# Kernel optimization log

Measured on AMD Instinct MI355X. Metric: run time of the kernel, lower is better.

Reference implementation:

```python
import jax, jax.numpy as jnp
import numpy as np

N, E = 100000, 3200000          # nodes, edges
D_IN, HID, OUT = 128, 128, 64   # in_channels, hidden_channels, out_channels
EPS = 1e-5                      # BatchNorm1d eps


def setup_inputs() -> dict:
    key = jax.random.key(0)
    ks = jax.random.split(key, 16)
    s = 0.05
    return {
        "x": jax.random.normal(ks[0], (N, D_IN), jnp.float32),
        "edge_index": jax.random.randint(ks[1], (2, E), 0, N, dtype=jnp.int64),
        # layer 0 (first_aggr=True): lin_pos_l (no bias), lin_pos_r (bias), lin_neg_r (bias)
        # (lin_neg_l acts on the all-zero neg aggregation -> contributes nothing, omitted)
        "w0_pos_l": jax.random.normal(ks[2], (HID, D_IN), jnp.float32) * s,
        "w0_pos_r": jax.random.normal(ks[3], (HID, D_IN), jnp.float32) * s,
        "b0_pos_r": jnp.zeros((HID,), jnp.float32),
        "w0_neg_r": jax.random.normal(ks[4], (HID, D_IN), jnp.float32) * s,
        "b0_neg_r": jnp.zeros((HID,), jnp.float32),
        # BatchNorm1d(2*HID)
        "bn_gamma": jnp.ones((2 * HID,), jnp.float32),
        "bn_beta": jnp.zeros((2 * HID,), jnp.float32),
        # layer 1 (first_aggr=False), in dim 2*HID split into pos/neg halves of HID.
        # Only the pos-edge aggregation block of lin_*_l is live (neg edges empty).
        "w1_pos_l": jax.random.normal(ks[5], (OUT, HID), jnp.float32) * s,
        "w1_pos_r": jax.random.normal(ks[6], (OUT, 2 * HID), jnp.float32) * s,
        "b1_pos_r": jnp.zeros((OUT,), jnp.float32),
        "w1_neg_l": jax.random.normal(ks[7], (OUT, HID), jnp.float32) * s,
        "w1_neg_r": jax.random.normal(ks[8], (OUT, 2 * HID), jnp.float32) * s,
        "b1_neg_r": jnp.zeros((OUT,), jnp.float32),
    }


def reference(x, edge_index, w0_pos_l, w0_pos_r, b0_pos_r, w0_neg_r, b0_neg_r,
              bn_gamma, bn_beta, w1_pos_l, w1_pos_r, b1_pos_r,
              w1_neg_l, w1_neg_r, b1_neg_r):
    src, dst = edge_index[0], edge_index[1]
    n = x.shape[0]
    deg = jax.ops.segment_sum(jnp.ones(src.shape, x.dtype), dst, num_segments=n)
    inv_deg = (1.0 / jnp.maximum(deg, 1.0))[:, None]

    def agg_mean(h):  # PyG mean aggregation over pos edges: src -> dst
        return jax.ops.segment_sum(h[src], dst, num_segments=n) * inv_deg

    # ---- layer 0: SignedConv(first_aggr=True); neg_edge_index is empty ----
    m = agg_mean(x)                                      # [N, D_IN]
    out_pos = m @ w0_pos_l.T + x @ w0_pos_r.T + b0_pos_r  # [N, HID]
    out_neg = x @ w0_neg_r.T + b0_neg_r                   # neg aggr == 0
    h = jnp.concatenate([out_pos, out_neg], axis=-1)      # [N, 2*HID]

    # ---- BatchNorm1d (batch statistics) + ReLU; dropout inactive (eval) ----
    mu = h.mean(axis=0)
    var = h.var(axis=0)
    h = (h - mu) * jax.lax.rsqrt(var + EPS) * bn_gamma + bn_beta
    h = jax.nn.relu(h)

    # ---- layer 1: SignedConv(first_aggr=False); neg edges empty ----
    f = h.shape[-1] // 2
    hp, hn = h[:, :f], h[:, f:]
    out_pos = agg_mean(hp) @ w1_pos_l.T + h @ w1_pos_r.T + b1_pos_r  # [N, OUT]
    out_neg = agg_mean(hn) @ w1_neg_l.T + h @ w1_neg_r.T + b1_neg_r  # [N, OUT]
    return jnp.concatenate([out_pos, out_neg], axis=-1)              # [N, 2*OUT]
```

## Files before the change

### kernel.cpp

```cpp
#include <hip/hip_runtime.h>
#include <stdint.h>

typedef __attribute__((ext_vector_type(8))) short short8;
typedef __attribute__((ext_vector_type(4))) float floatx4;

__device__ inline unsigned short f2bf(float f) {
    union { float f; unsigned u; } v; v.f = f;
    unsigned u = v.u;
    u += 0x7fffu + ((u >> 16) & 1u);
    return (unsigned short)(u >> 16);
}
__device__ inline unsigned char f2fp8(float f) {
    int r = __builtin_amdgcn_cvt_pk_fp8_f32(f, f, 0, false);
    return (unsigned char)(r & 0xff);
}

__global__ void k_detect(const unsigned* __restrict__ w, int* __restrict__ flag, int nwords) {
    unsigned a = 0;
    for (int i = 1 + 2 * (int)threadIdx.x; i < nwords; i += 512) a |= w[i];
    if (threadIdx.x == 0) *flag = 0;
    __syncthreads();
    if (a) *flag = 1;
}

__global__ void k_remap_hist(const void* __restrict__ ei_raw, const int* __restrict__ flag,
                             int* __restrict__ src, int* __restrict__ dst,
                             int* __restrict__ bhist, int E, int n, int NB) {
    __shared__ int lh[256];
    int t = threadIdx.x;
    if (t < 256) lh[t] = 0;
    __syncthreads();
    int base = blockIdx.x * 4096;
    bool is32 = (*flag != 0);
#pragma unroll
    for (int j = 0; j < 4; j++) {
        int e = base + j * 1024 + t;
        if (e < E) {
            int s, d;
            if (is32) { const int* p = (const int*)ei_raw; s = p[e]; d = p[E + e]; }
            else      { const long long* p = (const long long*)ei_raw; s = (int)p[e]; d = (int)p[E + e]; }
            s = s < 0 ? 0 : (s >= n ? n - 1 : s);
            d = d < 0 ? 0 : (d >= n ? n - 1 : d);
            src[e] = s; dst[e] = d;
            atomicAdd(&lh[d >> 9], 1);
        }
    }
    __syncthreads();
    if (t < NB && lh[t]) atomicAdd(&bhist[t], lh[t]);
}

__global__ void k_offsets(const int* __restrict__ bhist, int* __restrict__ bbase,
                          int* __restrict__ pcur, int* __restrict__ row_ptr,
                          int E, int n, int NB) {
    __shared__ int sc[256], orig[256];
    int t = threadIdx.x;
    int v = (t < NB) ? bhist[t] : 0;
    orig[t] = v; sc[t] = v;
    __syncthreads();
    for (int off = 1; off < 256; off <<= 1) {
        int x = (t >= off) ? sc[t - off] : 0;
        __syncthreads();
        sc[t] += x;
        __syncthreads();
    }
    if (t < NB) {
        int e = sc[t] - orig[t];
        bbase[t] = e; pcur[t] = e;
    }
    if (t == NB) bbase[t] = E;
    if (t == 0) row_ptr[n] = E;
}

__global__ void k_phase1(const int* __restrict__ src, const int* __restrict__ dst,
                         int* __restrict__ pcur, unsigned* __restrict__ pairs, int E, int NB) {
    __shared__ int lh[256];
    __shared__ int gbase[256];
    int t = threadIdx.x;
    if (t < 256) lh[t] = 0;
    __syncthreads();
    int base = blockIdx.x * 16384;
    int rank[16], dreg[16];
#pragma unroll
    for (int j = 0; j < 16; j++) {
        int e = base + j * 1024 + t;
        dreg[j] = -1;
        if (e < E) {
            int d = dst[e];
            dreg[j] = d;
            rank[j] = atomicAdd(&lh[d >> 9], 1);
        }
    }
    __syncthreads();
    if (t < NB && lh[t]) gbase[t] = atomicAdd(&pcur[t], lh[t]);
    __syncthreads();
#pragma unroll
    for (int j = 0; j < 16; j++) {
        int e = base + j * 1024 + t;
        if (e < E) {
            int s = src[e];
            int d = dreg[j];
            pairs[gbase[d >> 9] + rank[j]] = ((unsigned)s << 9) | (unsigned)(d & 511);
        }
    }
}

__global__ void k_phase2(const unsigned* __restrict__ pairs, const int* __restrict__ bbase,
                         int* __restrict__ row_ptr, float* __restrict__ inv_deg,
                         int* __restrict__ col, int n) {
    __shared__ int lcount[512];
    __shared__ int sc[512];
    __shared__ int lcur[512];
    int t = threadIdx.x;
    int b = blockIdx.x;
    lcount[t] = 0;
    __syncthreads();
    int e0 = bbase[b], e1 = bbase[b + 1];
    for (int i = e0 + t; i < e1; i += 512) {
        unsigned v = pairs[i];
        atomicAdd(&lcount[v & 511u], 1);
    }
    __syncthreads();
    sc[t] = lcount[t];
    __syncthreads();
    for (int off = 1; off < 512; off <<= 1) {
        int x = (t >= off) ? sc[t - off] : 0;
        __syncthreads();
        sc[t] += x;
        __syncthreads();
    }
    int excl = sc[t] - lcount[t];
    lcur[t] = excl;
    int g = b * 512 + t;
    if (g < n) {
        row_ptr[g] = e0 + excl;
        int c = lcount[t];
        inv_deg[g] = 1.0f / (float)(c > 1 ? c : 1);
    }
    __syncthreads();
    for (int i = e0 + t; i < e1; i += 512) {
        unsigned v = pairs[i];
        int f = v & 511u;
        int p = atomicAdd(&lcur[f], 1);
        col[e0 + p] = (int)(v >> 9);
    }
}

__global__ void k_w0prep(const float* __restrict__ wl, const float* __restrict__ wr,
                         const float* __restrict__ wn, unsigned short* __restrict__ W0f) {
    int tid = blockIdx.x * 256 + threadIdx.x;
    int lane = tid & 63; int ks = (tid >> 6) & 3; int ct = tid >> 8;
    int o = ct * 16 + (lane & 15);
    int k0 = ks * 32 + (lane >> 4) * 8;
    const float* sp = (o < 128) ? (wl + o * 128)
                    : (o < 256) ? (wr + (o - 128) * 128)
                                : (wn + (o - 256) * 128);
    union { unsigned short u[8]; short8 v; } pk;
#pragma unroll
    for (int j = 0; j < 8; j++) pk.u[j] = f2bf(sp[k0 + j]);
    ((short8*)W0f)[(ct * 4 + ks) * 64 + lane] = pk.v;
}

__global__ void k_w1prep(const float* __restrict__ wpl, const float* __restrict__ wnl,
                         const float* __restrict__ wpr, const float* __restrict__ wnr,
                         unsigned short* __restrict__ W1f) {
    int tid = blockIdx.x * 256 + threadIdx.x;
    int lane = tid & 63; int ks = (tid >> 6) & 7; int ct = tid >> 9;
    int o = ct * 16 + (lane & 15);
    int k0 = ks * 32 + (lane >> 4) * 8;
    union { unsigned short u[8]; short8 v; } pk;
#pragma unroll
    for (int j = 0; j < 8; j++) {
        int k = k0 + j;
        float v;
        if (o < 64)        v = (k < 128) ? wpl[o * 128 + k] : 0.0f;
        else if (o < 128)  v = (k >= 128) ? wnl[(o - 64) * 128 + (k - 128)] : 0.0f;
        else if (o < 192)  v = wpr[(o - 128) * 256 + k];
        else               v = wnr[(o - 192) * 256 + k];
        pk.u[j] = f2bf(v);
    }
    ((short8*)W1f)[(ct * 8 + ks) * 64 + lane] = pk.v;
}

__launch_bounds__(256, 2)
__global__ void k_gemm0(const float* __restrict__ x, const unsigned short* __restrict__ W0f,
                        const float* __restrict__ b0p, const float* __restrict__ b0n,
                        unsigned char* __restrict__ P, float* __restrict__ h, int n) {
    __shared__ unsigned short As[64 * 136];
    int t = threadIdx.x; int wave = t >> 6; int lane = t & 63;
    const short8* wf = (const short8*)W0f;
    short8 Bf[6][4];
#pragma unroll
    for (int i = 0; i < 6; i++) {
        int ct = wave * 6 + i;
#pragma unroll
        for (int ks = 0; ks < 4; ks++) Bf[i][ks] = wf[(ct * 4 + ks) * 64 + lane];
    }
    int rowbase = blockIdx.x * 64;
#pragma unroll
    for (int it = 0; it < 4; it++) {
        int seg = it * 256 + t;
        int r = seg >> 4; int k0 = (seg & 15) * 8;
        int row = rowbase + r;
        float4 a = {0, 0, 0, 0}, b = {0, 0, 0, 0};
        if (row < n) {
            a = *(const float4*)(x + (size_t)row * 128 + k0);
            b = *(const float4*)(x + (size_t)row * 128 + k0 + 4);
        }
        union { unsigned short u[8]; uint4 q; } pk;
        pk.u[0] = f2bf(a.x); pk.u[1] = f2bf(a.y); pk.u[2] = f2bf(a.z); pk.u[3] = f2bf(a.w);
        pk.u[4] = f2bf(b.x); pk.u[5] = f2bf(b.y); pk.u[6] = f2bf(b.z); pk.u[7] = f2bf(b.w);
        *(uint4*)(&As[r * 136 + k0]) = pk.q;
    }
    __syncthreads();
    int m = lane & 15; int quad = lane >> 4;
#pragma unroll
    for (int rt = 0; rt < 4; rt++) {
        floatx4 acc[6];
#pragma unroll
        for (int i = 0; i < 6; i++) acc[i] = (floatx4){0.f, 0.f, 0.f, 0.f};
#pragma unroll
        for (int ks = 0; ks < 4; ks++) {
            short8 a = *(const short8*)(&As[(rt * 16 + m) * 136 + ks * 32 + quad * 8]);
#pragma unroll
            for (int i = 0; i < 6; i++)
                acc[i] = __builtin_amdgcn_mfma_f32_16x16x32_bf16(a, Bf[i][ks], acc[i], 0, 0, 0);
        }
#pragma unroll
        for (int i = 0; i < 6; i++) {
            int colg = wave * 96 + i * 16 + m;
            float bias = 0.f;
            if (colg >= 128 && colg < 256) bias = b0p[colg - 128];
            else if (colg >= 256)          bias = b0n[colg - 256];
#pragma unroll
            for (int rr = 0; rr < 4; rr++) {
                int row = rowbase + rt * 16 + quad * 4 + rr;
                if (row < n) {
                    float v = acc[i][rr] + bias;
                    if (colg < 128) P[(size_t)row * 128 + colg] = f2fp8(v);
                    else            h[(size_t)row * 256 + (colg - 128)] = v;
                }
            }
        }
    }
}

template<int OSTRIDE>
__global__ __launch_bounds__(256) void k_agg(const int* __restrict__ row_ptr,
                                             const int* __restrict__ col,
                                             const float* __restrict__ inv_deg,
                                             const unsigned* __restrict__ Prow,
                                             float* __restrict__ out, int n) {
    int wid = threadIdx.x >> 6, lane = threadIdx.x & 63;
    int node = blockIdx.x * 4 + wid;
    if (node >= n) return;
    int e0 = row_ptr[node], e1 = row_ptr[node + 1];
    int half = lane >> 5, li = lane & 31;
    float a0 = 0.f, a1 = 0.f, a2 = 0.f, a3 = 0.f;
    for (int j = e0; j < e1; j += 64) {
        int cnt = e1 - j; if (cnt > 64) cnt = 64;
        int idx = j + lane;
        int myc = col[idx < e1 ? idx : e1 - 1];
        int i = 0;
        for (; i + 8 <= cnt; i += 8) {
            int sA = __shfl(myc, i + half);
            int sB = __shfl(myc, i + 2 + half);
            int sC = __shfl(myc, i + 4 + half);
            int sD = __shfl(myc, i + 6 + half);
            unsigned vA = Prow[(size_t)sA * 32 + li];
            unsigned vB = Prow[(size_t)sB * 32 + li];
            unsigned vC = Prow[(size_t)sC * 32 + li];
            unsigned vD = Prow[(size_t)sD * 32 + li];
            a0 += __builtin_amdgcn_cvt_f32_fp8(vA, 0); a1 += __builtin_amdgcn_cvt_f32_fp8(vA, 1);
            a2 += __builtin_amdgcn_cvt_f32_fp8(vA, 2); a3 += __builtin_amdgcn_cvt_f32_fp8(vA, 3);
            a0 += __builtin_amdgcn_cvt_f32_fp8(vB, 0); a1 += __builtin_amdgcn_cvt_f32_fp8(vB, 1);
            a2 += __builtin_amdgcn_cvt_f32_fp8(vB, 2); a3 += __builtin_amdgcn_cvt_f32_fp8(vB, 3);
            a0 += __builtin_amdgcn_cvt_f32_fp8(vC, 0); a1 += __builtin_amdgcn_cvt_f32_fp8(vC, 1);
            a2 += __builtin_amdgcn_cvt_f32_fp8(vC, 2); a3 += __builtin_amdgcn_cvt_f32_fp8(vC, 3);
            a0 += __builtin_amdgcn_cvt_f32_fp8(vD, 0); a1 += __builtin_amdgcn_cvt_f32_fp8(vD, 1);
            a2 += __builtin_amdgcn_cvt_f32_fp8(vD, 2); a3 += __builtin_amdgcn_cvt_f32_fp8(vD, 3);
        }
        for (; i + 2 <= cnt; i += 2) {
            int s = __shfl(myc, i + half);
            unsigned v = Prow[(size_t)s * 32 + li];
            a0 += __builtin_amdgcn_cvt_f32_fp8(v, 0); a1 += __builtin_amdgcn_cvt_f32_fp8(v, 1);
            a2 += __builtin_amdgcn_cvt_f32_fp8(v, 2); a3 += __builtin_amdgcn_cvt_f32_fp8(v, 3);
        }
        if (i < cnt) {
            int s = __shfl(myc, i);
            if (half == 0) {
                unsigned v = Prow[(size_t)s * 32 + li];
                a0 += __builtin_amdgcn_cvt_f32_fp8(v, 0); a1 += __builtin_amdgcn_cvt_f32_fp8(v, 1);
                a2 += __builtin_amdgcn_cvt_f32_fp8(v, 2); a3 += __builtin_amdgcn_cvt_f32_fp8(v, 3);
            }
        }
    }
    a0 += __shfl_xor(a0, 32);
    a1 += __shfl_xor(a1, 32);
    a2 += __shfl_xor(a2, 32);
    a3 += __shfl_xor(a3, 32);
    float idg = inv_deg[node];
    float rx = half ? a2 : a0;
    float ry = half ? a3 : a1;
    float* o = out + (size_t)node * OSTRIDE + 4 * li + 2 * half;
    float2 q = *(const float2*)o;
    float2 r;
    r.x = rx * idg + q.x;
    r.y = ry * idg + q.y;
    *(float2*)o = r;
}

__global__ void k_stats(const float* __restrict__ h, float* __restrict__ colsum,
                        float* __restrict__ colsumsq, int n) {
    int t = threadIdx.x;
    float s = 0.f, ss = 0.f;
    for (int r = blockIdx.x; r < n; r += gridDim.x) {
        float v = h[(size_t)r * 256 + t];
        s += v; ss += v * v;
    }
    atomicAdd(&colsum[t], s);
    atomicAdd(&colsumsq[t], ss);
}

__global__ void k_bnfin(const float* __restrict__ colsum, const float* __restrict__ colsumsq,
                        const float* __restrict__ gamma, const float* __restrict__ beta,
                        float* __restrict__ scale, float* __restrict__ shift, int n) {
    int t = threadIdx.x;
    float inv_n = 1.0f / (float)n;
    float mu = colsum[t] * inv_n;
    float var = colsumsq[t] * inv_n - mu * mu;
    float sc = gamma[t] * rsqrtf(var + 1e-5f);
    scale[t] = sc;
    shift[t] = beta[t] - mu * sc;
}

__launch_bounds__(256, 2)
__global__ void k_gemm1(const float* __restrict__ h, const unsigned short* __restrict__ W1f,
                        const float* __restrict__ bnscale, const float* __restrict__ bnshift,
                        const float* __restrict__ b1p, const float* __restrict__ b1n,
                        unsigned char* __restrict__ Y, float* __restrict__ out, int n) {
    __shared__ unsigned short As[64 * 264];
    __shared__ float sc[256], sh[256];
    int t = threadIdx.x; int wave = t >> 6; int lane = t & 63;
    sc[t] = bnscale[t]; sh[t] = bnshift[t];
    const short8* wf = (const short8*)W1f;
    short8 Bf[4][8];
#pragma unroll
    for (int i = 0; i < 4; i++) {
        int ct = wave * 4 + i;
#pragma unroll
        for (int ks = 0; ks < 8; ks++) Bf[i][ks] = wf[(ct * 8 + ks) * 64 + lane];
    }
    __syncthreads();
    int rowbase = blockIdx.x * 64;
#pragma unroll
    for (int it = 0; it < 8; it++) {
        int seg = it * 256 + t;
        int r = seg >> 5; int k0 = (seg & 31) * 8;
        int row = rowbase + r;
        union { unsigned short u[8]; uint4 q; } pk;
        if (row < n) {
            float4 a = *(const float4*)(h + (size_t)row * 256 + k0);
            float4 b = *(const float4*)(h + (size_t)row * 256 + k0 + 4);
            float vv[8] = {a.x, a.y, a.z, a.w, b.x, b.y, b.z, b.w};
#pragma unroll
            for (int q2 = 0; q2 < 8; q2++) {
                float v = vv[q2] * sc[k0 + q2] + sh[k0 + q2];
                v = v > 0.f ? v : 0.f;
                pk.u[q2] = f2bf(v);
            }
        } else {
#pragma unroll
            for (int q2 = 0; q2 < 8; q2++) pk.u[q2] = 0;
        }
        *(uint4*)(&As[r * 264 + k0]) = pk.q;
    }
    __syncthreads();
    int m = lane & 15; int quad = lane >> 4;
#pragma unroll
    for (int rt = 0; rt < 4; rt++) {
        floatx4 acc[4];
#pragma unroll
        for (int i = 0; i < 4; i++) acc[i] = (floatx4){0.f, 0.f, 0.f, 0.f};
#pragma unroll
        for (int ks = 0; ks < 8; ks++) {
            short8 a = *(const short8*)(&As[(rt * 16 + m) * 264 + ks * 32 + quad * 8]);
#pragma unroll
            for (int i = 0; i < 4; i++)
                acc[i] = __builtin_amdgcn_mfma_f32_16x16x32_bf16(a, Bf[i][ks], acc[i], 0, 0, 0);
        }
#pragma unroll
        for (int i = 0; i < 4; i++) {
            int colg = wave * 64 + i * 16 + m;
#pragma unroll
            for (int rr = 0; rr < 4; rr++) {
                int row = rowbase + rt * 16 + quad * 4 + rr;
                if (row < n) {
                    float v = acc[i][rr];
                    if (colg < 128) {
                        Y[(size_t)row * 128 + colg] = f2fp8(v);
                    } else {
                        float bias = (colg < 192) ? b1p[colg - 128] : b1n[colg - 192];
                        out[(size_t)row * 128 + (colg - 128)] = v + bias;
                    }
                }
            }
        }
    }
}

extern "C" void kernel_launch(void* const* d_in, const int* in_sizes, int n_in,
                              void* d_out, int out_size, void* d_ws, size_t ws_size,
                              hipStream_t stream) {
    const float* x        = (const float*)d_in[0];
    const void*  ei_raw   = d_in[1];
    const float* w0_pos_l = (const float*)d_in[2];
    const float* w0_pos_r = (const float*)d_in[3];
    const float* b0_pos_r = (const float*)d_in[4];
    const float* w0_neg_r = (const float*)d_in[5];
    const float* b0_neg_r = (const float*)d_in[6];
    const float* bn_gamma = (const float*)d_in[7];
    const float* bn_beta  = (const float*)d_in[8];
    const float* w1_pos_l = (const float*)d_in[9];
    const float* w1_pos_r = (const float*)d_in[10];
    const float* b1_pos_r = (const float*)d_in[11];
    const float* w1_neg_l = (const float*)d_in[12];
    const float* w1_neg_r = (const float*)d_in[13];
    const float* b1_neg_r = (const float*)d_in[14];
    float* out = (float*)d_out;
    int N = in_sizes[0] / 128;
    int E = in_sizes[1] / 2;
    int NB = (N + 511) >> 9;

    char* ws = (char*)d_ws;
    size_t off = 0;
    auto carve = [&](size_t bytes) -> char* {
        char* p = ws + off;
        off += (bytes + 255) & ~(size_t)255;
        return p;
    };
    int*      eflag   = (int*)carve(256);
    int*      src     = (int*)carve((size_t)E * 4);
    int*      dst     = (int*)carve((size_t)E * 4);
    int*      bhist   = (int*)carve((size_t)NB * 4);
    int*      bbase   = (int*)carve((size_t)(NB + 1) * 4);
    int*      pcur    = (int*)carve((size_t)NB * 4);
    int*      row_ptr = (int*)carve((size_t)(N + 1) * 4);
    float*    inv_deg = (float*)carve((size_t)N * 4);
    unsigned* pairs   = (unsigned*)carve((size_t)E * 4);
    int*      ecol    = (int*)carve((size_t)E * 4);
    unsigned char* P  = (unsigned char*)carve((size_t)N * 128);
    float* h          = (float*)carve((size_t)N * 256 * 4);
    unsigned char* Yb = (unsigned char*)carve((size_t)N * 128);
    unsigned short* W0f = (unsigned short*)carve(24 * 4 * 64 * 8 * 2);
    unsigned short* W1f = (unsigned short*)carve(16 * 8 * 64 * 8 * 2);
    float* colsum   = (float*)carve(2 * 256 * 4);
    float* colsumsq = colsum + 256;
    float* bnscale  = (float*)carve(256 * 4);
    float* bnshift  = (float*)carve(256 * 4);

    hipMemsetAsync(bhist, 0, (size_t)NB * 4, stream);
    hipMemsetAsync(colsum, 0, 2 * 256 * 4, stream);

    int nwords = 2 * E < 32768 ? 2 * E : 32768;
    k_detect<<<1, 256, 0, stream>>>((const unsigned*)ei_raw, eflag, nwords);
    k_remap_hist<<<(E + 4095) / 4096, 1024, 0, stream>>>(ei_raw, eflag, src, dst, bhist, E, N, NB);
    k_offsets<<<1, 256, 0, stream>>>(bhist, bbase, pcur, row_ptr, E, N, NB);
    k_phase1<<<(E + 16383) / 16384, 1024, 0, stream>>>(src, dst, pcur, pairs, E, NB);
    k_phase2<<<NB, 512, 0, stream>>>(pairs, bbase, row_ptr, inv_deg, ecol, N);

    k_w0prep<<<24, 256, 0, stream>>>(w0_pos_l, w0_pos_r, w0_neg_r, W0f);
    k_w1prep<<<32, 256, 0, stream>>>(w1_pos_l, w1_neg_l, w1_pos_r, w1_neg_r, W1f);

    int gb = (N + 63) / 64;
    k_gemm0<<<gb, 256, 0, stream>>>(x, W0f, b0_pos_r, b0_neg_r, P, h, N);
    k_agg<256><<<(N + 3) / 4, 256, 0, stream>>>(row_ptr, ecol, inv_deg, (const unsigned*)P, h, N);
    k_stats<<<256, 256, 0, stream>>>(h, colsum, colsumsq, N);
    k_bnfin<<<1, 256, 0, stream>>>(colsum, colsumsq, bn_gamma, bn_beta, bnscale, bnshift, N);
    k_gemm1<<<gb, 256, 0, stream>>>(h, W1f, bnscale, bnshift, b1_pos_r, b1_neg_r, Yb, out, N);
    k_agg<128><<<(N + 3) / 4, 256, 0, stream>>>(row_ptr, ecol, inv_deg, (const unsigned*)Yb, out, N);
}
```

Before: 606.6 us.

## Fuse BatchNorm column statistics into gemm0 and aggregation kernels

```diff
diff --git a/kernel.cpp b/kernel.cpp
--- a/kernel.cpp
+++ b/kernel.cpp
@@ -184,7 +184,8 @@
 __launch_bounds__(256, 2)
 __global__ void k_gemm0(const float* __restrict__ x, const unsigned short* __restrict__ W0f,
                         const float* __restrict__ b0p, const float* __restrict__ b0n,
-                        unsigned char* __restrict__ P, float* __restrict__ h, int n) {
+                        unsigned char* __restrict__ P, float* __restrict__ h,
+                        float* __restrict__ colsum, float* __restrict__ colsumsq, int n) {
     __shared__ unsigned short As[64 * 136];
     int t = threadIdx.x; int wave = t >> 6; int lane = t & 63;
     const short8* wf = (const short8*)W0f;
@@ -213,6 +214,9 @@
     }
     __syncthreads();
     int m = lane & 15; int quad = lane >> 4;
+    float cs[6], cq[6];
+#pragma unroll
+    for (int i = 0; i < 6; i++) { cs[i] = 0.f; cq[i] = 0.f; }
 #pragma unroll
     for (int rt = 0; rt < 4; rt++) {
         floatx4 acc[6];
@@ -236,89 +240,111 @@
                 int row = rowbase + rt * 16 + quad * 4 + rr;
                 if (row < n) {
                     float v = acc[i][rr] + bias;
-                    if (colg < 128) P[(size_t)row * 128 + colg] = f2fp8(v);
-                    else            h[(size_t)row * 256 + (colg - 128)] = v;
+                    if (colg < 128) {
+                        P[(size_t)row * 128 + colg] = f2fp8(v);
+                    } else {
+                        h[(size_t)row * 256 + (colg - 128)] = v;
+                        if (colg >= 256) { cs[i] += v; cq[i] += v * v; }
+                    }
                 }
             }
         }
     }
-}
-
-template<int OSTRIDE>
+#pragma unroll
+    for (int i = 0; i < 6; i++) {
+        int colg = wave * 96 + i * 16 + m;
+        if (colg >= 256) {
+            float s = cs[i];
+            s += __shfl_xor(s, 16); s += __shfl_xor(s, 32);
+            float q = cq[i];
+            q += __shfl_xor(q, 16); q += __shfl_xor(q, 32);
+            if (quad == 0) {
+                atomicAdd(&colsum[colg - 128], s);
+                atomicAdd(&colsumsq[colg - 128], q);
+            }
+        }
+    }
+}
+
+template<int OSTRIDE, bool STATS>
 __global__ __launch_bounds__(256) void k_agg(const int* __restrict__ row_ptr,
                                              const int* __restrict__ col,
                                              const float* __restrict__ inv_deg,
                                              const unsigned* __restrict__ Prow,
-                                             float* __restrict__ out, int n) {
+                                             float* __restrict__ out,
+                                             float* __restrict__ colsum,
+                                             float* __restrict__ colsumsq, int n) {
     int wid = threadIdx.x >> 6, lane = threadIdx.x & 63;
-    int node = blockIdx.x * 4 + wid;
-    if (node >= n) return;
-    int e0 = row_ptr[node], e1 = row_ptr[node + 1];
     int half = lane >> 5, li = lane & 31;
-    float a0 = 0.f, a1 = 0.f, a2 = 0.f, a3 = 0.f;
-    for (int j = e0; j < e1; j += 64) {
-        int cnt = e1 - j; if (cnt > 64) cnt = 64;
-        int idx = j + lane;
-        int myc = col[idx < e1 ? idx : e1 - 1];
-        int i = 0;
-        for (; i + 8 <= cnt; i += 8) {
-            int sA = __shfl(myc, i + half);
-            int sB = __shfl(myc, i + 2 + half);
-            int sC = __shfl(myc, i + 4 + half);
-            int sD = __shfl(myc, i + 6 + half);
-            unsigned vA = Prow[(size_t)sA * 32 + li];
-            unsigned vB = Prow[(size_t)sB * 32 + li];
-            unsigned vC = Prow[(size_t)sC * 32 + li];
-            unsigned vD = Prow[(size_t)sD * 32 + li];
-            a0 += __builtin_amdgcn_cvt_f32_fp8(vA, 0); a1 += __builtin_amdgcn_cvt_f32_fp8(vA, 1);
-            a2 += __builtin_amdgcn_cvt_f32_fp8(vA, 2); a3 += __builtin_amdgcn_cvt_f32_fp8(vA, 3);
-            a0 += __builtin_amdgcn_cvt_f32_fp8(vB, 0); a1 += __builtin_amdgcn_cvt_f32_fp8(vB, 1);
-            a2 += __builtin_amdgcn_cvt_f32_fp8(vB, 2); a3 += __builtin_amdgcn_cvt_f32_fp8(vB, 3);
-            a0 += __builtin_amdgcn_cvt_f32_fp8(vC, 0); a1 += __builtin_amdgcn_cvt_f32_fp8(vC, 1);
-            a2 += __builtin_amdgcn_cvt_f32_fp8(vC, 2); a3 += __builtin_amdgcn_cvt_f32_fp8(vC, 3);
-            a0 += __builtin_amdgcn_cvt_f32_fp8(vD, 0); a1 += __builtin_amdgcn_cvt_f32_fp8(vD, 1);
-            a2 += __builtin_amdgcn_cvt_f32_fp8(vD, 2); a3 += __builtin_amdgcn_cvt_f32_fp8(vD, 3);
-        }
-        for (; i + 2 <= cnt; i += 2) {
-            int s = __shfl(myc, i + half);
-            unsigned v = Prow[(size_t)s * 32 + li];
-            a0 += __builtin_amdgcn_cvt_f32_fp8(v, 0); a1 += __builtin_amdgcn_cvt_f32_fp8(v, 1);
-            a2 += __builtin_amdgcn_cvt_f32_fp8(v, 2); a3 += __builtin_amdgcn_cvt_f32_fp8(v, 3);
-        }
-        if (i < cnt) {
-            int s = __shfl(myc, i);
-            if (half == 0) {
+    float sx = 0.f, sy = 0.f, qx = 0.f, qy = 0.f;
+    for (int node = blockIdx.x * 4 + wid; node < n; node += gridDim.x * 4) {
+        int e0 = row_ptr[node], e1 = row_ptr[node + 1];
+        float a0 = 0.f, a1 = 0.f, a2 = 0.f, a3 = 0.f;
+        for (int j = e0; j < e1; j += 64) {
+            int cnt = e1 - j; if (cnt > 64) cnt = 64;
+            int idx = j + lane;
+            int myc = col[idx < e1 ? idx : e1 - 1];
+            int i = 0;
+            for (; i + 8 <= cnt; i += 8) {
+                int sA = __shfl(myc, i + half);
+                int sB = __shfl(myc, i + 2 + half);
+                int sC = __shfl(myc, i + 4 + half);
+                int sD = __shfl(myc, i + 6 + half);
+                unsigned vA = Prow[(size_t)sA * 32 + li];
+                unsigned vB = Prow[(size_t)sB * 32 + li];
+                unsigned vC = Prow[(size_t)sC * 32 + li];
+                unsigned vD = Prow[(size_t)sD * 32 + li];
+                a0 += __builtin_amdgcn_cvt_f32_fp8(vA, 0); a1 += __builtin_amdgcn_cvt_f32_fp8(vA, 1);
+                a2 += __builtin_amdgcn_cvt_f32_fp8(vA, 2); a3 += __builtin_amdgcn_cvt_f32_fp8(vA, 3);
+                a0 += __builtin_amdgcn_cvt_f32_fp8(vB, 0); a1 += __builtin_amdgcn_cvt_f32_fp8(vB, 1);
+                a2 += __builtin_amdgcn_cvt_f32_fp8(vB, 2); a3 += __builtin_amdgcn_cvt_f32_fp8(vB, 3);
+                a0 += __builtin_amdgcn_cvt_f32_fp8(vC, 0); a1 += __builtin_amdgcn_cvt_f32_fp8(vC, 1);
+                a2 += __builtin_amdgcn_cvt_f32_fp8(vC, 2); a3 += __builtin_amdgcn_cvt_f32_fp8(vC, 3);
+                a0 += __builtin_amdgcn_cvt_f32_fp8(vD, 0); a1 += __builtin_amdgcn_cvt_f32_fp8(vD, 1);
+                a2 += __builtin_amdgcn_cvt_f32_fp8(vD, 2); a3 += __builtin_amdgcn_cvt_f32_fp8(vD, 3);
+            }
+            for (; i + 2 <= cnt; i += 2) {
+                int s = __shfl(myc, i + half);
                 unsigned v = Prow[(size_t)s * 32 + li];
                 a0 += __builtin_amdgcn_cvt_f32_fp8(v, 0); a1 += __builtin_amdgcn_cvt_f32_fp8(v, 1);
                 a2 += __builtin_amdgcn_cvt_f32_fp8(v, 2); a3 += __builtin_amdgcn_cvt_f32_fp8(v, 3);
             }
-        }
-    }
-    a0 += __shfl_xor(a0, 32);
-    a1 += __shfl_xor(a1, 32);
-    a2 += __shfl_xor(a2, 32);
-    a3 += __shfl_xor(a3, 32);
-    float idg = inv_deg[node];
-    float rx = half ? a2 : a0;
-    float ry = half ? a3 : a1;
-    float* o = out + (size_t)node * OSTRIDE + 4 * li + 2 * half;
-    float2 q = *(const float2*)o;
-    float2 r;
-    r.x = rx * idg + q.x;
-    r.y = ry * idg + q.y;
-    *(float2*)o = r;
-}
-
-__global__ void k_stats(const float* __restrict__ h, float* __restrict__ colsum,
-                        float* __restrict__ colsumsq, int n) {
-    int t = threadIdx.x;
-    float s = 0.f, ss = 0.f;
-    for (int r = blockIdx.x; r < n; r += gridDim.x) {
-        float v = h[(size_t)r * 256 + t];
-        s += v; ss += v * v;
-    }
-    atomicAdd(&colsum[t], s);
-    atomicAdd(&colsumsq[t], ss);
+            if (i < cnt) {
+                int s = __shfl(myc, i);
+                if (half == 0) {
+                    unsigned v = Prow[(size_t)s * 32 + li];
+                    a0 += __builtin_amdgcn_cvt_f32_fp8(v, 0); a1 += __builtin_amdgcn_cvt_f32_fp8(v, 1);
+                    a2 += __builtin_amdgcn_cvt_f32_fp8(v, 2); a3 += __builtin_amdgcn_cvt_f32_fp8(v, 3);
+                }
+            }
+        }
+        a0 += __shfl_xor(a0, 32);
+        a1 += __shfl_xor(a1, 32);
+        a2 += __shfl_xor(a2, 32);
+        a3 += __shfl_xor(a3, 32);
+        float idg = inv_deg[node];
+        float rx = half ? a2 : a0;
+        float ry = half ? a3 : a1;
+        float* o = out + (size_t)node * OSTRIDE + 4 * li + 2 * half;
+        float2 q = *(const float2*)o;
+        float2 r;
+        r.x = rx * idg + q.x;
+        r.y = ry * idg + q.y;
+        *(float2*)o = r;
+        if (STATS) { sx += r.x; sy += r.y; qx += r.x * r.x; qy += r.y * r.y; }
+    }
+    if (STATS) {
+        __shared__ float S[4][128], Q[4][128];
+        int c0 = 4 * li + 2 * half;
+        S[wid][c0] = sx; S[wid][c0 + 1] = sy;
+        Q[wid][c0] = qx; Q[wid][c0 + 1] = qy;
+        __syncthreads();
+        int t = threadIdx.x;
+        if (t < 128) {
+            atomicAdd(&colsum[t], S[0][t] + S[1][t] + S[2][t] + S[3][t]);
+            atomicAdd(&colsumsq[t], Q[0][t] + Q[1][t] + Q[2][t] + Q[3][t]);
+        }
+    }
 }
 
 __global__ void k_bnfin(const float* __restrict__ colsum, const float* __restrict__ colsumsq,
@@ -472,10 +498,11 @@
     k_w1prep<<<32, 256, 0, stream>>>(w1_pos_l, w1_neg_l, w1_pos_r, w1_neg_r, W1f);
 
     int gb = (N + 63) / 64;
-    k_gemm0<<<gb, 256, 0, stream>>>(x, W0f, b0_pos_r, b0_neg_r, P, h, N);
-    k_agg<256><<<(N + 3) / 4, 256, 0, stream>>>(row_ptr, ecol, inv_deg, (const unsigned*)P, h, N);
-    k_stats<<<256, 256, 0, stream>>>(h, colsum, colsumsq, N);
+    k_gemm0<<<gb, 256, 0, stream>>>(x, W0f, b0_pos_r, b0_neg_r, P, h, colsum, colsumsq, N);
+    k_agg<256, true><<<2048, 256, 0, stream>>>(row_ptr, ecol, inv_deg, (const unsigned*)P, h,
+                                               colsum, colsumsq, N);
     k_bnfin<<<1, 256, 0, stream>>>(colsum, colsumsq, bn_gamma, bn_beta, bnscale, bnshift, N);
     k_gemm1<<<gb, 256, 0, stream>>>(h, W1f, bnscale, bnshift, b1_pos_r, b1_neg_r, Yb, out, N);
-    k_agg<128><<<(N + 3) / 4, 256, 0, stream>>>(row_ptr, ecol, inv_deg, (const unsigned*)Yb, out, N);
-}
+    k_agg<128, false><<<2048, 256, 0, stream>>>(row_ptr, ecol, inv_deg, (const unsigned*)Yb, out,
+                                                nullptr, nullptr, N);
+}
```

Measured after the change: 564.1 us. 7.0% less time.
